# Kernel optimization log

Measured on AMD Instinct MI355X. Metric: run time of the kernel, lower is better.

Reference implementation:

```python
import jax, jax.numpy as jnp
import numpy as np

LN2 = 0.6931471805599453

def ssp(x):
    # 'shifted_sp' activation: softplus(x) - log(2)
    return jax.nn.softplus(x) - LN2

def _res_chain(x, W1, b1, W2, b2):
    # PhysNetResidual chain: x <- lin2(ssp(lin1(ssp(x)))) + x
    # W1/W2: [n_res, F, F], b1/b2: [n_res, F]
    for j in range(W1.shape[0]):
        h = ssp(x) @ W1[j] + b1[j]
        x = ssp(h) @ W2[j] + b2[j] + x
    return x

def _physnet_module(feat, radial_aev, idx12, p):
    (W_I, b_I, W_J, b_J, W_gate, gvec, W_int, b_int,
     ri_W1, ri_b1, ri_W2, ri_b2,
     ra_W1, ra_b1, ra_W2, ra_b2,
     ro_W1, ro_b1, ro_W2, ro_b2, W_out, b_out) = p
    N, F = feat.shape
    # self term (no species are dummy -> non_dummy indexing is identity)
    h_self = ssp(ssp(feat) @ W_I + b_I)                       # [N,F]
    # pair messages
    gate = radial_aev @ W_gate                                 # [P,F] (no bias)
    f12 = feat[idx12]                                          # [2,P,F] gather
    fm = ssp(ssp(f12) @ W_J + b_J)                             # [2,P,F]
    pair_msg = gate[None] * fm                                 # [2,P,F]
    proto = jnp.zeros_like(feat).at[idx12.reshape(-1)].add(
        pair_msg.reshape(-1, F))                               # scatter-add
    proto = proto + h_self
    msg = _res_chain(proto, ri_W1, ri_b1, ri_W2, ri_b2)
    feat2 = feat * gvec + ssp(msg) @ W_int + b_int
    feat2 = _res_chain(feat2, ra_W1, ra_b1, ra_W2, ra_b2)
    e = ssp(_res_chain(feat2, ro_W1, ro_b1, ro_W2, ro_b2)) @ W_out + b_out  # [N]
    return e, feat2

def setup_inputs() -> dict:
    key = jax.random.key(0)
    L, F, R = 5, 128, 64
    M, A = 128, 64
    N = M * A
    P = 400000
    ks = jax.random.split(key, 20)
    s = 0.05  # small weight scale keeps activations stable across 5 modules
    inp = {
        'species': jax.random.randint(ks[0], (M, A), 0, 4, dtype=jnp.int32),
        'features': jax.random.normal(ks[1], (N, F), jnp.float32),
        'radial_aev': jax.random.uniform(ks[2], (P, R), jnp.float32),
        'atom_index12': jax.random.randint(ks[3], (2, P), 0, N, dtype=jnp.int32),
        'W_I': jax.random.normal(ks[4], (L, F, F)) * s,
        'b_I': jnp.zeros((L, F)),
        'W_J': jax.random.normal(ks[5], (L, F, F)) * s,
        'b_J': jnp.zeros((L, F)),
        'W_gate': jax.random.normal(ks[6], (L, R, F)) * s,
        'gvec': jnp.ones((L, F)),
        'W_int': jax.random.normal(ks[7], (L, F, F)) * s,
        'b_int': jnp.zeros((L, F)),
        'ri_W1': jax.random.normal(ks[8], (L, 3, F, F)) * s,
        'ri_b1': jnp.zeros((L, 3, F)),
        'ri_W2': jax.random.normal(ks[9], (L, 3, F, F)) * s,
        'ri_b2': jnp.zeros((L, 3, F)),
        'ra_W1': jax.random.normal(ks[10], (L, 2, F, F)) * s,
        'ra_b1': jnp.zeros((L, 2, F)),
        'ra_W2': jax.random.normal(ks[11], (L, 2, F, F)) * s,
        'ra_b2': jnp.zeros((L, 2, F)),
        'ro_W1': jax.random.normal(ks[12], (L, 1, F, F)) * s,
        'ro_b1': jnp.zeros((L, 1, F)),
        'ro_W2': jax.random.normal(ks[13], (L, 1, F, F)) * s,
        'ro_b2': jnp.zeros((L, 1, F)),
        'W_out': jax.random.normal(ks[14], (L, F)) * s,
        'b_out': jnp.zeros((L,)),
    }
    return inp

def reference(species, features, radial_aev, atom_index12,
              W_I, b_I, W_J, b_J, W_gate, gvec, W_int, b_int,
              ri_W1, ri_b1, ri_W2, ri_b2,
              ra_W1, ra_b1, ra_W2, ra_b2,
              ro_W1, ro_b1, ro_W2, ro_b2, W_out, b_out):
    M, A = species.shape
    params = (W_I, b_I, W_J, b_J, W_gate, gvec, W_int, b_int,
              ri_W1, ri_b1, ri_W2, ri_b2,
              ra_W1, ra_b1, ra_W2, ra_b2,
              ro_W1, ro_b1, ro_W2, ro_b2, W_out, b_out)
    feat = features
    energies = jnp.zeros((M * A,), features.dtype)
    for l in range(W_I.shape[0]):  # fixed small module loop
        p = tuple(arr[l] for arr in params)
        e, feat = _physnet_module(feat, radial_aev, atom_index12, p)
        energies = energies + e
    return energies.reshape(M, A), feat
```

## Files before the change

kernel.cpp:

```cpp
#include <hip/hip_runtime.h>


#define LN2F 0.69314718055994530942f
#define NB 128

using short8  = __attribute__((ext_vector_type(8))) short;
using float4v = __attribute__((ext_vector_type(4))) float;
typedef const __attribute__((address_space(1))) unsigned int* gas1_t;
typedef __attribute__((address_space(3))) unsigned int* las3_t;

__device__ __forceinline__ float sspf(float x) {
  float ax = fabsf(x);
  return fmaxf(x, 0.0f) + __logf(1.0f + __expf(-ax)) - LN2F;
}

__device__ __forceinline__ unsigned short f2bf(float x) {
  return (unsigned short)((__float_as_uint(x) + 0x8000u) >> 16);
}

__device__ __forceinline__ unsigned short f2bf_ne(float x) {
  unsigned int u = __float_as_uint(x);
  u += 0x7fffu + ((u >> 16) & 1u);
  return (unsigned short)(u >> 16);
}

__device__ __forceinline__ void dma16(const void* g, void* l) {
  __builtin_amdgcn_global_load_lds((gas1_t)(unsigned long long)g,
                                   (las3_t)(unsigned long long)l, 16, 0, 0);
}

__device__ __forceinline__ void dma32k(const unsigned short* g, unsigned short* l,
                                       int w, int lane) {
  const char* gb = (const char*)g + w * 2048 + lane * 16;
  char* lb = (char*)l + w * 2048;
  dma16(gb, lb);
  dma16(gb + 1024, lb + 1024);
}
__device__ __forceinline__ void dma16k(const unsigned short* g, unsigned short* l,
                                       int w, int lane) {
  dma16((const char*)g + w * 1024 + lane * 16, (char*)l + w * 1024);
}

__global__ __launch_bounds__(256) void hist_pass(const int* __restrict__ idx,
                                                 unsigned int* __restrict__ H,
                                                 int n2p, int C) {
  __shared__ unsigned int h[8192];
  int b = blockIdx.x, tid = threadIdx.x;
  for (int i = tid; i < 8192; i += 256) h[i] = 0;
  __syncthreads();
  int s = b * C, e = min(s + C, n2p);
  for (int i = s + tid; i < e; i += 256) atomicAdd(&h[idx[i]], 1u);
  __syncthreads();
  for (int i = tid; i < 8192; i += 256) H[(size_t)b * 8192 + i] = h[i];
}

__global__ __launch_bounds__(256) void col_scan(unsigned int* __restrict__ H,
                                                unsigned int* __restrict__ tot) {
  int a = blockIdx.x * 256 + threadIdx.x;
  unsigned int run = 0;
  for (int b = 0; b < NB; ++b) {
    unsigned int v = H[(size_t)b * 8192 + a];
    H[(size_t)b * 8192 + a] = run;
    run += v;
  }
  tot[a] = run;
}

__global__ __launch_bounds__(256) void scan_kernel(const unsigned int* __restrict__ cnt,
                                                   unsigned int* __restrict__ off, int NA) {
  int t = threadIdx.x;
  unsigned int local[32], s = 0;
#pragma unroll
  for (int i = 0; i < 32; ++i) { local[i] = cnt[t * 32 + i]; s += local[i]; }
  unsigned int v = s;
  int lane = t & 63, w = t >> 6;
#pragma unroll
  for (int o = 1; o < 64; o <<= 1) {
    unsigned int u = __shfl_up(v, o, 64);
    if (lane >= o) v += u;
  }
  __shared__ unsigned int wt4[4];
  if (lane == 63) wt4[w] = v;
  __syncthreads();
  unsigned int base = 0;
  for (int k = 0; k < w; ++k) base += wt4[k];
  unsigned int excl = base + v - s;
#pragma unroll
  for (int i = 0; i < 32; ++i) { off[t * 32 + i] = excl; excl += local[i]; }
  if (t == 255) off[NA] = excl;
}

__global__ __launch_bounds__(256) void place_pass(const int* __restrict__ idx,
                                                  const unsigned int* __restrict__ H,
                                                  const unsigned int* __restrict__ off,
                                                  unsigned int* __restrict__ pairid,
                                                  int P, int C) {
  __shared__ unsigned int pos[8192];
  int b = blockIdx.x, tid = threadIdx.x;
  for (int i = tid; i < 8192; i += 256)
    pos[i] = off[i] + H[(size_t)b * 8192 + i];
  __syncthreads();
  int n2p = 2 * P;
  int s = b * C, e = min(s + C, n2p);
  for (int i = s + tid; i < e; i += 256) {
    int a = idx[i];
    unsigned int p = atomicAdd(&pos[a], 1u);
    pairid[p] = (i >= P) ? (unsigned int)(i - P) : (unsigned int)i;
  }
}

__global__ __launch_bounds__(256) void gather_kernel(const float* __restrict__ radial,
                                                     const unsigned int* __restrict__ off,
                                                     const unsigned int* __restrict__ pairid,
                                                     float* __restrict__ S) {
  __shared__ float red[3][64];
  int a = blockIdx.x;
  int lane = threadIdx.x & 63, w = threadIdx.x >> 6;
  unsigned int b = off[a], e = off[a + 1];
  float acc = 0.0f;
  for (unsigned int base = b + w; base < e; base += 32) {
    unsigned int pp[8];
    float vv[8];
#pragma unroll
    for (int k = 0; k < 8; ++k) {
      unsigned int j = base + 4 * k;
      pp[k] = pairid[j < e ? j : b];
    }
#pragma unroll
    for (int k = 0; k < 8; ++k) vv[k] = radial[(size_t)pp[k] * 64 + lane];
#pragma unroll
    for (int k = 0; k < 8; ++k) {
      unsigned int j = base + 4 * k;
      acc += (j < e) ? vv[k] : 0.0f;
    }
  }
  if (w > 0) red[w - 1][lane] = acc;
  __syncthreads();
  if (w == 0) {
    acc += red[0][lane] + red[1][lane] + red[2][lane];
    S[(size_t)a * 64 + lane] = acc;
  }
}

struct PrepArgs {
  const float* src[80];
  int isgate[80];
};

__global__ __launch_bounds__(256) void prep_weights(PrepArgs A, unsigned short* __restrict__ Wt) {
  int m = blockIdx.x;
  const float* s = A.src[m];
  unsigned short* d = Wt + (size_t)m * 16384;
  if (!A.isgate[m]) {
    for (int it = 0; it < 8; ++it) {
      int q = threadIdx.x + it * 256;
      int n = q & 127, j = q >> 7;
      unsigned short tmp[8];
#pragma unroll
      for (int cc = 0; cc < 8; ++cc) tmp[cc] = f2bf_ne(s[(8 * j + cc) * 128 + n]);
      *(uint4*)(d + (n * 16 + (j ^ (n & 15))) * 8) = *(uint4*)tmp;
    }
  } else {
    for (int it = 0; it < 4; ++it) {
      int q = threadIdx.x + it * 256;
      int n = q & 127, j = q >> 7;
      unsigned short tmp[8];
#pragma unroll
      for (int cc = 0; cc < 8; ++cc) tmp[cc] = f2bf_ne(s[(8 * j + cc) * 128 + n]);
      *(uint4*)(d + (n * 8 + (j ^ (n & 7))) * 8) = *(uint4*)tmp;
    }
  }
}

struct BiasArgs {
  const float* p[17];
  int stride[17];
  const float* b_out;
};

__global__ __launch_bounds__(256) void pack_bias(BiasArgs B, float* __restrict__ dst) {
  int l = blockIdx.x;
  for (int i = threadIdx.x; i < 17 * 128; i += 256) {
    int s = i >> 7;
    dst[(size_t)l * 2304 + i] = B.p[s][l * B.stride[s] + (i & 127)];
  }
  if (threadIdx.x == 0) dst[(size_t)l * 2304 + 17 * 128] = B.b_out[l];
}

struct ChainArgs {
  const float* feat_in;
  const float* S;
  const unsigned short* wt;
  const float* bias_pack;
  float* feat_out;
  float* energy;
};

__device__ __forceinline__ void gemm128s(const unsigned short* sA_, const unsigned short* sW,
                                         int arow, int col0, int l16, int quad, float4v* acc) {
  const unsigned short* ar = sA_ + (arow + l16) * 136 + quad * 8;
  short8 a0 = *(const short8*)(ar);
  short8 a1 = *(const short8*)(ar + 32);
  short8 a2 = *(const short8*)(ar + 64);
  short8 a3 = *(const short8*)(ar + 96);
  const unsigned short* bb = sW + col0 * 128;
  *acc = __builtin_amdgcn_mfma_f32_16x16x32_bf16(a0, *(const short8*)(bb + ((quad + 0) ^ l16) * 8), *acc, 0, 0, 0);
  *acc = __builtin_amdgcn_mfma_f32_16x16x32_bf16(a1, *(const short8*)(bb + ((quad + 4) ^ l16) * 8), *acc, 0, 0, 0);
  *acc = __builtin_amdgcn_mfma_f32_16x16x32_bf16(a2, *(const short8*)(bb + ((quad + 8) ^ l16) * 8), *acc, 0, 0, 0);
  *acc = __builtin_amdgcn_mfma_f32_16x16x32_bf16(a3, *(const short8*)(bb + ((quad + 12) ^ l16) * 8), *acc, 0, 0, 0);
}

__device__ __forceinline__ void gemm64s(const unsigned short* sS_, const unsigned short* sW,
                                        int arow, int col0, int l16, int quad, float4v* acc) {
  const unsigned short* ar = sS_ + (arow + l16) * 72 + quad * 8;
  short8 a0 = *(const short8*)(ar);
  short8 a1 = *(const short8*)(ar + 32);
  int l8 = l16 & 7;
  const unsigned short* bb = sW + col0 * 64;
  *acc = __builtin_amdgcn_mfma_f32_16x16x32_bf16(a0, *(const short8*)(bb + ((quad + 0) ^ l8) * 8), *acc, 0, 0, 0);
  *acc = __builtin_amdgcn_mfma_f32_16x16x32_bf16(a1, *(const short8*)(bb + ((quad + 4) ^ l8) * 8), *acc, 0, 0, 0);
}

__device__ __forceinline__ void write_ssp_A(unsigned short* sA_, const float4v v,
                                            int arow, int col0, int quad) {
#pragma unroll
  for (int r = 0; r < 4; ++r)
    sA_[(arow + quad * 4 + r) * 136 + col0] = f2bf(sspf(v[r]));
}

__global__ __launch_bounds__(1024, 4) void chain_kernel(ChainArgs A) {
  __shared__ __align__(16) unsigned short swb[2][16384];
  __shared__ __align__(16) unsigned short sA[2][32 * 136];
  __shared__ __align__(16) unsigned short sS[32 * 72];
  __shared__ float sBias[2304];
  __shared__ float sE[32];

  const int tid  = threadIdx.x;
  const int row0 = blockIdx.x * 32;
  const int lane = tid & 63;
  const int w    = tid >> 6;
  const int g    = w >> 3;
  const int c    = w & 7;
  const int l16  = lane & 15;
  const int quad = lane >> 4;
  const int arow = 16 * g;
  const int col0 = 16 * c + l16;

  dma16k(A.wt, swb[0], w, lane);

  for (int i = tid; i < 32 * 64; i += 1024) {
    int r = i >> 6, k = i & 63;
    sS[r * 72 + k] = f2bf(A.S[(size_t)(row0 + r) * 64 + k]);
  }
  for (int i = tid; i < 32 * 128; i += 1024) {
    int r = i >> 7, k = i & 127;
    sA[0][r * 136 + k] = f2bf(sspf(A.feat_in[(size_t)(row0 + r) * 128 + k]));
  }
  float4v ff;
#pragma unroll
  for (int r = 0; r < 4; ++r)
    ff[r] = A.feat_in[(size_t)(row0 + arow + quad * 4 + r) * 128 + col0];
  if (tid < 32) sE[tid] = 0.0f;
  __syncthreads();

  const float4v Z = {0.f, 0.f, 0.f, 0.f};
  float4v gG, fm, xf, t4;
  float p0 = 0.f, p1 = 0.f, p2 = 0.f, p3 = 0.f, bsum = 0.f;

#pragma unroll 1
  for (int l = 0; l < 5; ++l) {
    const size_t slot0 = (size_t)l * 16 * 16384;

    dma32k(A.wt + slot0 + 16384, swb[1], w, lane);
    for (int i = tid; i < 2304; i += 1024) sBias[i] = A.bias_pack[(size_t)l * 2304 + i];
    gG = Z;
    gemm64s(sS, swb[0], arow, col0, l16, quad, &gG);
    __syncthreads();

    dma32k(A.wt + slot0 + 2 * 16384, swb[0], w, lane);
    fm = Z;
    gemm128s(sA[0], swb[1], arow, col0, l16, quad, &fm);
    {
      float bv = sBias[0 * 128 + col0];
#pragma unroll
      for (int r = 0; r < 4; ++r) fm[r] = sspf(fm[r] + bv);
    }
    __syncthreads();

    dma32k(A.wt + slot0 + 3 * 16384, swb[1], w, lane);
    t4 = Z;
    gemm128s(sA[0], swb[0], arow, col0, l16, quad, &t4);
    {
      float bv = sBias[1 * 128 + col0];
#pragma unroll
      for (int r = 0; r < 4; ++r) xf[r] = fm[r] * gG[r] + sspf(t4[r] + bv);
    }
    write_ssp_A(sA[1], xf, arow, col0, quad);
    __syncthreads();

#pragma unroll
    for (int jj = 0; jj < 3; ++jj) {
      const int th = 3 + 2 * jj;
      dma32k(A.wt + slot0 + (size_t)(th + 1) * 16384, swb[th & 1 ? 0 : 1], w, lane);
      t4 = Z;
      gemm128s(sA[1], swb[th & 1], arow, col0, l16, quad, &t4);
      {
        float bv = sBias[(th - 1) * 128 + col0];
#pragma unroll
        for (int r = 0; r < 4; ++r) t4[r] += bv;
      }
      write_ssp_A(sA[0], t4, arow, col0, quad);
      __syncthreads();

      const int tx = th + 1;
      dma32k(A.wt + slot0 + (size_t)(tx + 1) * 16384, swb[tx & 1 ? 0 : 1], w, lane);
      t4 = Z;
      gemm128s(sA[0], swb[tx & 1], arow, col0, l16, quad, &t4);
      {
        float bv = sBias[(tx - 1) * 128 + col0];
#pragma unroll
        for (int r = 0; r < 4; ++r) xf[r] += t4[r] + bv;
      }
      write_ssp_A(sA[1], xf, arow, col0, quad);
      __syncthreads();
    }

    dma32k(A.wt + slot0 + 10 * 16384, swb[0], w, lane);
    t4 = Z;
    gemm128s(sA[1], swb[1], arow, col0, l16, quad, &t4);
    {
      float bv = sBias[8 * 128 + col0];
      float gv = sBias[15 * 128 + col0];
#pragma unroll
      for (int r = 0; r < 4; ++r) xf[r] = ff[r] * gv + t4[r] + bv;
    }
    write_ssp_A(sA[0], xf, arow, col0, quad);
    __syncthreads();

#pragma unroll
    for (int jj = 0; jj < 2; ++jj) {
      const int th = 10 + 2 * jj;
      dma32k(A.wt + slot0 + (size_t)(th + 1) * 16384, swb[th & 1 ? 0 : 1], w, lane);
      t4 = Z;
      gemm128s(sA[0], swb[th & 1], arow, col0, l16, quad, &t4);
      {
        float bv = sBias[(th - 1) * 128 + col0];
#pragma unroll
        for (int r = 0; r < 4; ++r) t4[r] += bv;
      }
      write_ssp_A(sA[1], t4, arow, col0, quad);
      __syncthreads();

      const int tx = th + 1;
      dma32k(A.wt + slot0 + (size_t)(tx + 1) * 16384, swb[tx & 1 ? 0 : 1], w, lane);
      t4 = Z;
      gemm128s(sA[1], swb[tx & 1], arow, col0, l16, quad, &t4);
      {
        float bv = sBias[(tx - 1) * 128 + col0];
#pragma unroll
        for (int r = 0; r < 4; ++r) xf[r] += t4[r] + bv;
      }
      write_ssp_A(sA[0], xf, arow, col0, quad);
      __syncthreads();
    }

    ff = xf;
    if (l == 4) {
#pragma unroll
      for (int r = 0; r < 4; ++r)
        A.feat_out[(size_t)(row0 + arow + quad * 4 + r) * 128 + col0] = xf[r];
    }

    dma32k(A.wt + slot0 + 15 * 16384, swb[1], w, lane);
    t4 = Z;
    gemm128s(sA[0], swb[0], arow, col0, l16, quad, &t4);
    {
      float bv = sBias[13 * 128 + col0];
#pragma unroll
      for (int r = 0; r < 4; ++r) t4[r] += bv;
    }
    write_ssp_A(sA[1], t4, arow, col0, quad);
    __syncthreads();

    if (l < 4) dma16k(A.wt + slot0 + 16 * 16384, swb[0], w, lane);
    t4 = Z;
    gemm128s(sA[1], swb[1], arow, col0, l16, quad, &t4);
    {
      float bv = sBias[14 * 128 + col0];
      float wv = sBias[16 * 128 + col0];
      p0 += sspf(xf[0] + t4[0] + bv) * wv;
      p1 += sspf(xf[1] + t4[1] + bv) * wv;
      p2 += sspf(xf[2] + t4[2] + bv) * wv;
      p3 += sspf(xf[3] + t4[3] + bv) * wv;
    }
    bsum += sBias[17 * 128];
    __syncthreads();
  }

#pragma unroll
  for (int o = 1; o < 16; o <<= 1) {
    p0 += __shfl_xor(p0, o, 64);
    p1 += __shfl_xor(p1, o, 64);
    p2 += __shfl_xor(p2, o, 64);
    p3 += __shfl_xor(p3, o, 64);
  }
  if (l16 == 0) {
    atomicAdd(&sE[arow + quad * 4 + 0], p0);
    atomicAdd(&sE[arow + quad * 4 + 1], p1);
    atomicAdd(&sE[arow + quad * 4 + 2], p2);
    atomicAdd(&sE[arow + quad * 4 + 3], p3);
  }
  __syncthreads();
  if (tid < 32) A.energy[row0 + tid] = sE[tid] + bsum;
}

extern "C" void kernel_launch(void* const* d_in, const int* in_sizes, int n_in,
                              void* d_out, int out_size, void* d_ws, size_t ws_size,
                              hipStream_t stream) {
  const float* features = (const float*)d_in[1];
  const float* radial   = (const float*)d_in[2];
  const int*   idx12    = (const int*)  d_in[3];
  const float* W_I    = (const float*)d_in[4];
  const float* b_I    = (const float*)d_in[5];
  const float* W_J    = (const float*)d_in[6];
  const float* b_J    = (const float*)d_in[7];
  const float* W_gate = (const float*)d_in[8];
  const float* gvec   = (const float*)d_in[9];
  const float* W_int  = (const float*)d_in[10];
  const float* b_int  = (const float*)d_in[11];
  const float* ri_W1  = (const float*)d_in[12];
  const float* ri_b1  = (const float*)d_in[13];
  const float* ri_W2  = (const float*)d_in[14];
  const float* ri_b2  = (const float*)d_in[15];
  const float* ra_W1  = (const float*)d_in[16];
  const float* ra_b1  = (const float*)d_in[17];
  const float* ra_W2  = (const float*)d_in[18];
  const float* ra_b2  = (const float*)d_in[19];
  const float* ro_W1  = (const float*)d_in[20];
  const float* ro_b1  = (const float*)d_in[21];
  const float* ro_W2  = (const float*)d_in[22];
  const float* ro_b2  = (const float*)d_in[23];
  const float* W_out  = (const float*)d_in[24];
  const float* b_out  = (const float*)d_in[25];

  const int N = in_sizes[1] / 128;
  const int P = in_sizes[3] / 2;
  const int L = in_sizes[25];
  const int n2p = 2 * P;
  const int C = (n2p + NB - 1) / NB;

  float* S = (float*)d_ws;
  float* bias_pack = S + (size_t)N * 64;
  unsigned short* Wt = (unsigned short*)(bias_pack + 5 * 2304);
  unsigned int* H      = (unsigned int*)(Wt + (size_t)80 * 16384);
  unsigned int* tot    = H + (size_t)NB * 8192;
  unsigned int* off    = tot + N;
  unsigned int* pairid = off + N + 4;

  PrepArgs pa;
  for (int l = 0; l < L; ++l) {
    const float* fx[16] = {
      W_gate + l * 8192,
      W_J + l * 16384, W_I + l * 16384,
      ri_W1 + (l * 3 + 0) * 16384, ri_W2 + (l * 3 + 0) * 16384,
      ri_W1 + (l * 3 + 1) * 16384, ri_W2 + (l * 3 + 1) * 16384,
      ri_W1 + (l * 3 + 2) * 16384, ri_W2 + (l * 3 + 2) * 16384,
      W_int + l * 16384,
      ra_W1 + (l * 2 + 0) * 16384, ra_W2 + (l * 2 + 0) * 16384,
      ra_W1 + (l * 2 + 1) * 16384, ra_W2 + (l * 2 + 1) * 16384,
      ro_W1 + l * 16384, ro_W2 + l * 16384 };
    for (int t = 0; t < 16; ++t) { pa.src[l * 16 + t] = fx[t]; pa.isgate[l * 16 + t] = (t == 0); }
  }
  prep_weights<<<80, 256, 0, stream>>>(pa, Wt);

  BiasArgs ba;
  const float* bp[17] = { b_J, b_I,
    ri_b1, ri_b2, ri_b1 + 128, ri_b2 + 128, ri_b1 + 256, ri_b2 + 256,
    b_int, ra_b1, ra_b2, ra_b1 + 128, ra_b2 + 128, ro_b1, ro_b2, gvec, W_out };
  int st[17] = {128,128, 384,384,384,384,384,384, 128, 256,256,256,256, 128,128,128,128};
  for (int q = 0; q < 17; ++q) { ba.p[q] = bp[q]; ba.stride[q] = st[q]; }
  ba.b_out = b_out;
  pack_bias<<<5, 256, 0, stream>>>(ba, bias_pack);

  hist_pass<<<NB, 256, 0, stream>>>(idx12, H, n2p, C);
  col_scan<<<32, 256, 0, stream>>>(H, tot);
  scan_kernel<<<1, 256, 0, stream>>>(tot, off, N);
  place_pass<<<NB, 256, 0, stream>>>(idx12, H, off, pairid, P, C);
  gather_kernel<<<N, 256, 0, stream>>>(radial, off, pairid, S);

  ChainArgs ca;
  ca.feat_in   = features;
  ca.S         = S;
  ca.wt        = Wt;
  ca.bias_pack = bias_pack;
  ca.energy    = (float*)d_out;
  ca.feat_out  = (float*)d_out + N;
  chain_kernel<<<N / 32, 1024, 0, stream>>>(ca);
}
```

Measured before the change: 349.5 us.

## Fuse weight/bias prep kernels, halve histogram blocks, stage col_scan in LDS, precompute LDS offsets

Merges the weight conversion and bias packing into one launch and splits each weight matrix across two blocks. Halves the number of histogram blocks and has col_scan stage its column in shared memory before scanning. In the chain kernel, LDS byte offsets are computed once per thread and passed to the GEMM helpers instead of recomputing the address arithmetic. Fewer histogram blocks means less parallelism in hist_pass and place_pass, each block handling twice the pairs.

After: 359.9 us. +3.0%, slower.

```diff
diff --git a/kernel.cpp b/kernel.cpp
--- a/kernel.cpp
+++ b/kernel.cpp
@@ -2,7 +2,7 @@
 
 
 #define LN2F 0.69314718055994530942f
-#define NB 128
+#define NB 64
 
 using short8  = __attribute__((ext_vector_type(8))) short;
 using float4v = __attribute__((ext_vector_type(4))) float;
@@ -56,14 +56,23 @@
 
 __global__ __launch_bounds__(256) void col_scan(unsigned int* __restrict__ H,
                                                 unsigned int* __restrict__ tot) {
-  int a = blockIdx.x * 256 + threadIdx.x;
+  __shared__ unsigned int h[NB * 256];
+  int t = threadIdx.x;
+  size_t cb = (size_t)blockIdx.x * 256;
+#pragma unroll 4
+  for (int b = 0; b < NB; ++b) h[b * 256 + t] = H[(size_t)b * 8192 + cb + t];
+  __syncthreads();
   unsigned int run = 0;
+#pragma unroll
   for (int b = 0; b < NB; ++b) {
-    unsigned int v = H[(size_t)b * 8192 + a];
-    H[(size_t)b * 8192 + a] = run;
+    unsigned int v = h[b * 256 + t];
+    h[b * 256 + t] = run;
     run += v;
   }
-  tot[a] = run;
+  __syncthreads();
+#pragma unroll 4
+  for (int b = 0; b < NB; ++b) H[(size_t)b * 8192 + cb + t] = h[b * 256 + t];
+  tot[cb + t] = run;
 }
 
 __global__ __launch_bounds__(256) void scan_kernel(const unsigned int* __restrict__ cnt,
@@ -142,17 +151,31 @@
   }
 }
 
-struct PrepArgs {
+struct PrepAll {
   const float* src[80];
   int isgate[80];
+  const float* bp[17];
+  int stride[17];
+  const float* b_out;
 };
 
-__global__ __launch_bounds__(256) void prep_weights(PrepArgs A, unsigned short* __restrict__ Wt) {
-  int m = blockIdx.x;
+__global__ __launch_bounds__(256) void prep_all(PrepAll A, unsigned short* __restrict__ Wt,
+                                                float* __restrict__ bias_pack) {
+  int bid = blockIdx.x;
+  if (bid >= 160) {
+    int l = bid - 160;
+    for (int i = threadIdx.x; i < 17 * 128; i += 256) {
+      int s = i >> 7;
+      bias_pack[(size_t)l * 2304 + i] = A.bp[s][l * A.stride[s] + (i & 127)];
+    }
+    if (threadIdx.x == 0) bias_pack[(size_t)l * 2304 + 17 * 128] = A.b_out[l];
+    return;
+  }
+  int m = bid >> 1, half = bid & 1;
   const float* s = A.src[m];
   unsigned short* d = Wt + (size_t)m * 16384;
   if (!A.isgate[m]) {
-    for (int it = 0; it < 8; ++it) {
+    for (int it = half * 4; it < half * 4 + 4; ++it) {
       int q = threadIdx.x + it * 256;
       int n = q & 127, j = q >> 7;
       unsigned short tmp[8];
@@ -161,7 +184,7 @@
       *(uint4*)(d + (n * 16 + (j ^ (n & 15))) * 8) = *(uint4*)tmp;
     }
   } else {
-    for (int it = 0; it < 4; ++it) {
+    for (int it = half * 2; it < half * 2 + 2; ++it) {
       int q = threadIdx.x + it * 256;
       int n = q & 127, j = q >> 7;
       unsigned short tmp[8];
@@ -170,21 +193,6 @@
       *(uint4*)(d + (n * 8 + (j ^ (n & 7))) * 8) = *(uint4*)tmp;
     }
   }
-}
-
-struct BiasArgs {
-  const float* p[17];
-  int stride[17];
-  const float* b_out;
-};
-
-__global__ __launch_bounds__(256) void pack_bias(BiasArgs B, float* __restrict__ dst) {
-  int l = blockIdx.x;
-  for (int i = threadIdx.x; i < 17 * 128; i += 256) {
-    int s = i >> 7;
-    dst[(size_t)l * 2304 + i] = B.p[s][l * B.stride[s] + (i & 127)];
-  }
-  if (threadIdx.x == 0) dst[(size_t)l * 2304 + 17 * 128] = B.b_out[l];
 }
 
 struct ChainArgs {
@@ -196,41 +204,43 @@
   float* energy;
 };
 
-__device__ __forceinline__ void gemm128s(const unsigned short* sA_, const unsigned short* sW,
-                                         int arow, int col0, int l16, int quad, float4v* acc) {
-  const unsigned short* ar = sA_ + (arow + l16) * 136 + quad * 8;
-  short8 a0 = *(const short8*)(ar);
-  short8 a1 = *(const short8*)(ar + 32);
-  short8 a2 = *(const short8*)(ar + 64);
-  short8 a3 = *(const short8*)(ar + 96);
-  const unsigned short* bb = sW + col0 * 128;
-  *acc = __builtin_amdgcn_mfma_f32_16x16x32_bf16(a0, *(const short8*)(bb + ((quad + 0) ^ l16) * 8), *acc, 0, 0, 0);
-  *acc = __builtin_amdgcn_mfma_f32_16x16x32_bf16(a1, *(const short8*)(bb + ((quad + 4) ^ l16) * 8), *acc, 0, 0, 0);
-  *acc = __builtin_amdgcn_mfma_f32_16x16x32_bf16(a2, *(const short8*)(bb + ((quad + 8) ^ l16) * 8), *acc, 0, 0, 0);
-  *acc = __builtin_amdgcn_mfma_f32_16x16x32_bf16(a3, *(const short8*)(bb + ((quad + 12) ^ l16) * 8), *acc, 0, 0, 0);
-}
-
-__device__ __forceinline__ void gemm64s(const unsigned short* sS_, const unsigned short* sW,
-                                        int arow, int col0, int l16, int quad, float4v* acc) {
-  const unsigned short* ar = sS_ + (arow + l16) * 72 + quad * 8;
-  short8 a0 = *(const short8*)(ar);
-  short8 a1 = *(const short8*)(ar + 32);
-  int l8 = l16 & 7;
-  const unsigned short* bb = sW + col0 * 64;
-  *acc = __builtin_amdgcn_mfma_f32_16x16x32_bf16(a0, *(const short8*)(bb + ((quad + 0) ^ l8) * 8), *acc, 0, 0, 0);
-  *acc = __builtin_amdgcn_mfma_f32_16x16x32_bf16(a1, *(const short8*)(bb + ((quad + 4) ^ l8) * 8), *acc, 0, 0, 0);
-}
-
-__device__ __forceinline__ void write_ssp_A(unsigned short* sA_, const float4v v,
-                                            int arow, int col0, int quad) {
+#define MFMA16(a, b, acc) __builtin_amdgcn_mfma_f32_16x16x32_bf16(a, b, acc, 0, 0, 0)
+
+__device__ __forceinline__ void gemm128o(const unsigned short* sAb, const unsigned short* swbb,
+                                         unsigned as, unsigned ws,
+                                         const unsigned aO[4], const unsigned bO[4],
+                                         float4v* acc) {
+  const char* ab = (const char*)sAb + as;
+  const char* wb = (const char*)swbb + ws;
+  short8 a0 = *(const short8*)(ab + aO[0]);
+  short8 a1 = *(const short8*)(ab + aO[1]);
+  short8 a2 = *(const short8*)(ab + aO[2]);
+  short8 a3 = *(const short8*)(ab + aO[3]);
+  *acc = MFMA16(a0, *(const short8*)(wb + bO[0]), *acc);
+  *acc = MFMA16(a1, *(const short8*)(wb + bO[1]), *acc);
+  *acc = MFMA16(a2, *(const short8*)(wb + bO[2]), *acc);
+  *acc = MFMA16(a3, *(const short8*)(wb + bO[3]), *acc);
+}
+
+__device__ __forceinline__ void gemm64o(const unsigned short* sSb, const unsigned short* swbb,
+                                        unsigned s0, unsigned s1, unsigned g0, unsigned g1,
+                                        float4v* acc) {
+  short8 a0 = *(const short8*)((const char*)sSb + s0);
+  short8 a1 = *(const short8*)((const char*)sSb + s1);
+  *acc = MFMA16(a0, *(const short8*)((const char*)swbb + g0), *acc);
+  *acc = MFMA16(a1, *(const short8*)((const char*)swbb + g1), *acc);
+}
+
+__device__ __forceinline__ void wsspo(unsigned short* sAb, unsigned as,
+                                      const unsigned wO[4], const float4v v) {
 #pragma unroll
   for (int r = 0; r < 4; ++r)
-    sA_[(arow + quad * 4 + r) * 136 + col0] = f2bf(sspf(v[r]));
+    *(unsigned short*)((char*)sAb + as + wO[r]) = f2bf(sspf(v[r]));
 }
 
 __global__ __launch_bounds__(1024, 4) void chain_kernel(ChainArgs A) {
-  __shared__ __align__(16) unsigned short swb[2][16384];
-  __shared__ __align__(16) unsigned short sA[2][32 * 136];
+  __shared__ __align__(16) unsigned short swb[2 * 16384];
+  __shared__ __align__(16) unsigned short sA[2 * 32 * 136];
   __shared__ __align__(16) unsigned short sS[32 * 72];
   __shared__ float sBias[2304];
   __shared__ float sE[32];
@@ -245,8 +255,21 @@
   const int quad = lane >> 4;
   const int arow = 16 * g;
   const int col0 = 16 * c + l16;
-
-  dma16k(A.wt, swb[0], w, lane);
+  const int l8   = l16 & 7;
+
+  unsigned aO[4], bO[4], wO[4];
+#pragma unroll
+  for (int k = 0; k < 4; ++k) {
+    aO[k] = (unsigned)(((arow + l16) * 136 + quad * 8 + k * 32) * 2);
+    bO[k] = (unsigned)((col0 * 128 + ((quad + 4 * k) ^ l16) * 8) * 2);
+    wO[k] = (unsigned)(((arow + quad * 4 + k) * 136 + col0) * 2);
+  }
+  const unsigned sO0 = (unsigned)(((arow + l16) * 72 + quad * 8) * 2);
+  const unsigned sO1 = sO0 + 64;
+  const unsigned gO0 = (unsigned)((col0 * 64 + ((quad + 0) ^ l8) * 8) * 2);
+  const unsigned gO1 = (unsigned)((col0 * 64 + ((quad + 4) ^ l8) * 8) * 2);
+
+  dma16k(A.wt, swb, w, lane);
 
   for (int i = tid; i < 32 * 64; i += 1024) {
     int r = i >> 6, k = i & 63;
@@ -254,7 +277,7 @@
   }
   for (int i = tid; i < 32 * 128; i += 1024) {
     int r = i >> 7, k = i & 127;
-    sA[0][r * 136 + k] = f2bf(sspf(A.feat_in[(size_t)(row0 + r) * 128 + k]));
+    sA[r * 136 + k] = f2bf(sspf(A.feat_in[(size_t)(row0 + r) * 128 + k]));
   }
   float4v ff;
 #pragma unroll
@@ -271,15 +294,15 @@
   for (int l = 0; l < 5; ++l) {
     const size_t slot0 = (size_t)l * 16 * 16384;
 
-    dma32k(A.wt + slot0 + 16384, swb[1], w, lane);
+    dma32k(A.wt + slot0 + 16384, swb + 16384, w, lane);
     for (int i = tid; i < 2304; i += 1024) sBias[i] = A.bias_pack[(size_t)l * 2304 + i];
     gG = Z;
-    gemm64s(sS, swb[0], arow, col0, l16, quad, &gG);
+    gemm64o(sS, swb, sO0, sO1, gO0, gO1, &gG);
     __syncthreads();
 
-    dma32k(A.wt + slot0 + 2 * 16384, swb[0], w, lane);
+    dma32k(A.wt + slot0 + 2 * 16384, swb, w, lane);
     fm = Z;
-    gemm128s(sA[0], swb[1], arow, col0, l16, quad, &fm);
+    gemm128o(sA, swb, 0, 32768, aO, bO, &fm);
     {
       float bv = sBias[0 * 128 + col0];
 #pragma unroll
@@ -287,80 +310,80 @@
     }
     __syncthreads();
 
-    dma32k(A.wt + slot0 + 3 * 16384, swb[1], w, lane);
+    dma32k(A.wt + slot0 + 3 * 16384, swb + 16384, w, lane);
     t4 = Z;
-    gemm128s(sA[0], swb[0], arow, col0, l16, quad, &t4);
+    gemm128o(sA, swb, 0, 0, aO, bO, &t4);
     {
       float bv = sBias[1 * 128 + col0];
 #pragma unroll
       for (int r = 0; r < 4; ++r) xf[r] = fm[r] * gG[r] + sspf(t4[r] + bv);
     }
-    write_ssp_A(sA[1], xf, arow, col0, quad);
+    wsspo(sA, 8704, wO, xf);
     __syncthreads();
 
 #pragma unroll
     for (int jj = 0; jj < 3; ++jj) {
       const int th = 3 + 2 * jj;
-      dma32k(A.wt + slot0 + (size_t)(th + 1) * 16384, swb[th & 1 ? 0 : 1], w, lane);
+      dma32k(A.wt + slot0 + (size_t)(th + 1) * 16384, swb, w, lane);
       t4 = Z;
-      gemm128s(sA[1], swb[th & 1], arow, col0, l16, quad, &t4);
+      gemm128o(sA, swb, 8704, 32768, aO, bO, &t4);
       {
         float bv = sBias[(th - 1) * 128 + col0];
 #pragma unroll
         for (int r = 0; r < 4; ++r) t4[r] += bv;
       }
-      write_ssp_A(sA[0], t4, arow, col0, quad);
+      wsspo(sA, 0, wO, t4);
       __syncthreads();
 
       const int tx = th + 1;
-      dma32k(A.wt + slot0 + (size_t)(tx + 1) * 16384, swb[tx & 1 ? 0 : 1], w, lane);
+      dma32k(A.wt + slot0 + (size_t)(tx + 1) * 16384, swb + 16384, w, lane);
       t4 = Z;
-      gemm128s(sA[0], swb[tx & 1], arow, col0, l16, quad, &t4);
+      gemm128o(sA, swb, 0, 0, aO, bO, &t4);
       {
         float bv = sBias[(tx - 1) * 128 + col0];
 #pragma unroll
         for (int r = 0; r < 4; ++r) xf[r] += t4[r] + bv;
       }
-      write_ssp_A(sA[1], xf, arow, col0, quad);
+      wsspo(sA, 8704, wO, xf);
       __syncthreads();
     }
 
-    dma32k(A.wt + slot0 + 10 * 16384, swb[0], w, lane);
+    dma32k(A.wt + slot0 + 10 * 16384, swb, w, lane);
     t4 = Z;
-    gemm128s(sA[1], swb[1], arow, col0, l16, quad, &t4);
+    gemm128o(sA, swb, 8704, 32768, aO, bO, &t4);
     {
       float bv = sBias[8 * 128 + col0];
       float gv = sBias[15 * 128 + col0];
 #pragma unroll
       for (int r = 0; r < 4; ++r) xf[r] = ff[r] * gv + t4[r] + bv;
     }
-    write_ssp_A(sA[0], xf, arow, col0, quad);
+    wsspo(sA, 0, wO, xf);
     __syncthreads();
 
 #pragma unroll
     for (int jj = 0; jj < 2; ++jj) {
       const int th = 10 + 2 * jj;
-      dma32k(A.wt + slot0 + (size_t)(th + 1) * 16384, swb[th & 1 ? 0 : 1], w, lane);
+      dma32k(A.wt + slot0 + (size_t)(th + 1) * 16384, swb + 16384, w, lane);
       t4 = Z;
-      gemm128s(sA[0], swb[th & 1], arow, col0, l16, quad, &t4);
+      gemm128o(sA, swb, 0, 0, aO, bO, &t4);
       {
         float bv = sBias[(th - 1) * 128 + col0];
 #pragma unroll
         for (int r = 0; r < 4; ++r) t4[r] += bv;
       }
-      write_ssp_A(sA[1], t4, arow, col0, quad);
+      wsspo(sA, 8704, wO, t4);
       __syncthreads();
 
       const int tx = th + 1;
-      dma32k(A.wt + slot0 + (size_t)(tx + 1) * 16384, swb[tx & 1 ? 0 : 1], w, lane);
+      dma32k(A.wt + slot0 + (size_t)(tx + 1) * 16384, swb, w, lane);
       t4 = Z;
-      gemm128s(sA[1], swb[tx & 1], arow, col0, l16, quad, &t4);
+      gemm128o(sA, swb, 8704, 32768, aO, bO, &t4);
       {
         float bv = sBias[(tx - 1) * 128 + col0];
 #pragma unroll
         for (int r = 0; r < 4; ++r) xf[r] += t4[r] + bv;
       }
-      write_ssp_A(sA[0], xf, arow, col0, quad);
+      wsspo(sA, 0, wO, xf);
       __syncthreads();
     }
 
@@ -371,20 +394,20 @@
         A.feat_out[(size_t)(row0 + arow + quad * 4 + r) * 128 + col0] = xf[r];
     }
 
-    dma32k(A.wt + slot0 + 15 * 16384, swb[1], w, lane);
+    dma32k(A.wt + slot0 + 15 * 16384, swb + 16384, w, lane);
     t4 = Z;
-    gemm128s(sA[0], swb[0], arow, col0, l16, quad, &t4);
+    gemm128o(sA, swb, 0, 0, aO, bO, &t4);
     {
       float bv = sBias[13 * 128 + col0];
 #pragma unroll
       for (int r = 0; r < 4; ++r) t4[r] += bv;
     }
-    write_ssp_A(sA[1], t4, arow, col0, quad);
+    wsspo(sA, 8704, wO, t4);
     __syncthreads();
 
-    if (l < 4) dma16k(A.wt + slot0 + 16 * 16384, swb[0], w, lane);
+    if (l < 4) dma16k(A.wt + slot0 + 16 * 16384, swb, w, lane);
     t4 = Z;
-    gemm128s(sA[1], swb[1], arow, col0, l16, quad, &t4);
+    gemm128o(sA, swb, 8704, 32768, aO, bO, &t4);
     {
       float bv = sBias[14 * 128 + col0];
       float wv = sBias[16 * 128 + col0];
@@ -457,7 +480,7 @@
   unsigned int* off    = tot + N;
   unsigned int* pairid = off + N + 4;
 
-  PrepArgs pa;
+  PrepAll pa;
   for (int l = 0; l < L; ++l) {
     const float* fx[16] = {
       W_gate + l * 8192,
@@ -471,16 +494,13 @@
       ro_W1 + l * 16384, ro_W2 + l * 16384 };
     for (int t = 0; t < 16; ++t) { pa.src[l * 16 + t] = fx[t]; pa.isgate[l * 16 + t] = (t == 0); }
   }
-  prep_weights<<<80, 256, 0, stream>>>(pa, Wt);
-
-  BiasArgs ba;
   const float* bp[17] = { b_J, b_I,
     ri_b1, ri_b2, ri_b1 + 128, ri_b2 + 128, ri_b1 + 256, ri_b2 + 256,
     b_int, ra_b1, ra_b2, ra_b1 + 128, ra_b2 + 128, ro_b1, ro_b2, gvec, W_out };
   int st[17] = {128,128, 384,384,384,384,384,384, 128, 256,256,256,256, 128,128,128,128};
-  for (int q = 0; q < 17; ++q) { ba.p[q] = bp[q]; ba.stride[q] = st[q]; }
-  ba.b_out = b_out;
-  pack_bias<<<5, 256, 0, stream>>>(ba, bias_pack);
+  for (int q = 0; q < 17; ++q) { pa.bp[q] = bp[q]; pa.stride[q] = st[q]; }
+  pa.b_out = b_out;
+  prep_all<<<165, 256, 0, stream>>>(pa, Wt, bias_pack);
 
   hist_pass<<<NB, 256, 0, stream>>>(idx12, H, n2p, C);
   col_scan<<<32, 256, 0, stream>>>(H, tot);
```
